# Kernel tuning notes

Measured on AMD Instinct MI355X. Metric: run time of the kernel, lower is better.

The kernel has to match this reference:

```python
import jax, jax.numpy as jnp
import numpy as np

N_HEAD = 16
N_KV_HEAD = 4
WINDOW = 256
ROPE_BASE = 10000.0


def _rotate_half(x):
    h = x.shape[-1] // 2
    return jnp.concatenate([-x[..., h:], x[..., :h]], axis=-1)


def _rope_cos_sin(T, D):
    inv_freq = 1.0 / (ROPE_BASE ** (jnp.arange(0, D, 2, dtype=jnp.float32) / D))
    t = jnp.arange(T, dtype=jnp.float32)
    freqs = t[:, None] * inv_freq[None, :]            # [T, D/2]
    emb = jnp.concatenate([freqs, freqs], axis=-1)    # [T, D]
    return jnp.cos(emb)[None, None], jnp.sin(emb)[None, None]  # [1,1,T,D]


def _masks(T, w):
    tq = jnp.arange(T)
    tk = jnp.arange(T)
    causal = tk[None, :] <= tq[:, None]
    i_blk = (tq // w) * w                              # window block start per query
    k_start = jnp.maximum(0, i_blk - w // 2)           # local key slice start
    # torch SDPA is_causal with L!=S: top-left aligned tril -> local kj <= local qi
    upper = tq - (i_blk - k_start)
    local = (tk[None, :] >= k_start[:, None]) & (tk[None, :] <= upper[:, None])
    return causal, local


def setup_inputs() -> dict:
    key = jax.random.key(0)
    k0, k1, k2, k3, k4 = jax.random.split(key, 5)
    B, T, C = 1, 2048, 2048
    D = C // N_HEAD
    s = 0.02
    return {
        "x": jax.random.normal(k0, (B, T, C), dtype=jnp.float32),
        "wq": jax.random.normal(k1, (C, N_HEAD * D), dtype=jnp.float32) * s,
        "wk": jax.random.normal(k2, (C, N_KV_HEAD * D), dtype=jnp.float32) * s,
        "wv": jax.random.normal(k3, (C, N_KV_HEAD * D), dtype=jnp.float32) * s,
        "wo": jax.random.normal(k4, (C, C), dtype=jnp.float32) * s,
    }


def reference(x, wq, wk, wv, wo):
    B, T, C = x.shape
    D = C // N_HEAD
    g = N_HEAD // N_KV_HEAD

    q = (x @ wq).reshape(B, T, N_HEAD, D)
    k = (x @ wk).reshape(B, T, N_KV_HEAD, D)
    v = (x @ wv).reshape(B, T, N_KV_HEAD, D)
    k = jnp.repeat(k, g, axis=2)                       # GQA repeat_interleave
    v = jnp.repeat(v, g, axis=2)
    q = q.transpose(0, 2, 1, 3)                        # [B,H,T,D]
    k = k.transpose(0, 2, 1, 3)
    v = v.transpose(0, 2, 1, 3)

    cos, sin = _rope_cos_sin(T, D)
    q = q * cos + _rotate_half(q) * sin
    k = k * cos + _rotate_half(k) * sin

    scale = 1.0 / jnp.sqrt(jnp.asarray(D, dtype=q.dtype))
    scores = jnp.einsum('bhqd,bhkd->bhqk', q, k) * scale
    causal, local = _masks(T, WINDOW)
    neg = jnp.finfo(scores.dtype).min
    p_g = jax.nn.softmax(jnp.where(causal, scores, neg), axis=-1)
    p_l = jax.nn.softmax(jnp.where(local, scores, neg), axis=-1)
    out_g = jnp.einsum('bhqk,bhkd->bhqd', p_g, v)
    out_l = jnp.einsum('bhqk,bhkd->bhqd', p_l, v)
    out = 0.5 * (out_g + out_l)
    out = out.transpose(0, 2, 1, 3).reshape(B, T, C)
    return out @ wo
```

## Files before the change

kernel.cpp:

```cpp
#include <hip/hip_runtime.h>
#include <hip/hip_bf16.h>
#include <cstdint>
#include <cstddef>

#define T_SEQ 2048
#define CDIM  2048
#define HQ    16
#define HKV   4
#define DHEAD 128
#define NQKV  3072

typedef __bf16 bf8 __attribute__((ext_vector_type(8)));
typedef __bf16 bf4 __attribute__((ext_vector_type(4)));
typedef float  f4  __attribute__((ext_vector_type(4)));

static __device__ __forceinline__ f4 mfma16(bf8 a, bf8 b, f4 c) {
    return __builtin_amdgcn_mfma_f32_16x16x32_bf16(a, b, c, 0, 0, 0);
}

#define GLOAD16(g, l)                                                        \
    __builtin_amdgcn_global_load_lds(                                        \
        (const __attribute__((address_space(1))) void*)(g),                  \
        (__attribute__((address_space(3))) void*)(l), 16, 0, 0)

__global__ __launch_bounds__(256) void k_pre(const float* __restrict__ x,
                                             const float* __restrict__ wq,
                                             const float* __restrict__ wk,
                                             const float* __restrict__ wv,
                                             const float* __restrict__ wo,
                                             __bf16* __restrict__ xbf,
                                             float* __restrict__ tab,
                                             __bf16* __restrict__ wqkvT,
                                             __bf16* __restrict__ woT) {
    const int bid = blockIdx.x, tid = threadIdx.x;
    if (bid < 4096) {
        int i = bid * 256 + tid;
        float4 v = ((const float4*)x)[i];
        bf4 o;
        o[0] = (__bf16)v.x; o[1] = (__bf16)v.y; o[2] = (__bf16)v.z; o[3] = (__bf16)v.w;
        ((bf4*)xbf)[i] = o;
        return;
    }
    if (bid < 4608) {
        int idx = (bid - 4096) * 256 + tid;
        int t = idx >> 6, j = idx & 63;
        float invf = expf(-(float)j * (9.210340371976184f / 64.0f));
        float a = (float)t * invf;
        tab[idx * 2 + 0] = cosf(a);
        tab[idx * 2 + 1] = sinf(a);
        return;
    }
    __shared__ float tile[32][33];
    const int n = bid - 4608;
    const int bx = n % 160, by = n / 160;
    const float* src; __bf16* dst; int ld_src, cx;
    if (bx < 64)      { src = wq; dst = wqkvT;                        ld_src = 2048; cx = bx; }
    else if (bx < 80) { src = wk; dst = wqkvT + (size_t)2048 * 2048;  ld_src = 512;  cx = bx - 64; }
    else if (bx < 96) { src = wv; dst = wqkvT + (size_t)2560 * 2048;  ld_src = 512;  cx = bx - 80; }
    else              { src = wo; dst = woT;                          ld_src = 2048; cx = bx - 96; }
    const int c0 = cx * 32, r0 = by * 32;
    const int tx = tid & 31, ty = tid >> 5;
#pragma unroll
    for (int i = 0; i < 4; ++i)
        tile[ty + i * 8][tx] = src[(size_t)(r0 + ty + i * 8) * ld_src + c0 + tx];
    __syncthreads();
#pragma unroll
    for (int i = 0; i < 4; ++i)
        dst[(size_t)(c0 + ty + i * 8) * 2048 + r0 + tx] = (__bf16)tile[tx][ty + i * 8];
}

template <int MODE>
__global__ __launch_bounds__(512, 4) void k_gemm(const __bf16* __restrict__ A,
                                                 const __bf16* __restrict__ BT,
                                                 float* __restrict__ C,
                                                 const float2* __restrict__ tab,
                                                 __bf16* __restrict__ Qo,
                                                 __bf16* __restrict__ Ko,
                                                 __bf16* __restrict__ Vo,
                                                 int M, int N, int K) {
    __shared__ __bf16 lds[2][2][128 * 64];
    char* L = (char*)&lds[0][0][0];
    const int tid = threadIdx.x, wid = tid >> 6, lane = tid & 63;
    const int l15 = lane & 15, lhi = lane >> 4;
    const int wr = wid >> 1, wc = wid & 1;
    const size_t arow0 = (size_t)blockIdx.y * 128;
    const size_t brow0 = (size_t)blockIdx.x * 128;

    const int sr = tid >> 3;
    const int sc8 = ((tid & 7) ^ ((tid >> 3) & 7)) * 8;
    const __bf16* Ag = A + (arow0 + sr) * K + sc8;
    const __bf16* Bg = BT + (brow0 + sr) * K + sc8;

#define GSTAGE(buf, k0)                                                          \
    {                                                                            \
        _Pragma("unroll") for (int i = 0; i < 2; ++i) {                          \
            GLOAD16(Ag + (k0) + (size_t)i * 64 * K,                              \
                    L + (buf) * 32768 + i * 8192 + tid * 16);                    \
            GLOAD16(Bg + (k0) + (size_t)i * 64 * K,                              \
                    L + (buf) * 32768 + 16384 + i * 8192 + tid * 16);            \
        }                                                                        \
    }

    f4 acc[2][4] = {};
    GSTAGE(0, 0);
    __syncthreads();
    int cur = 0;

    for (int k0 = 0; k0 < K; k0 += 64) {
        if (k0 + 64 < K) GSTAGE(cur ^ 1, k0 + 64);
        const char* Ab = L + cur * 32768;
        const char* Bb = Ab + 16384;
        bf8 af[2][2], bfr[2][4];
#pragma unroll
        for (int kk = 0; kk < 2; ++kk) {
            const int ch = ((kk * 4 + lhi) ^ (l15 & 7)) * 16;
#pragma unroll
            for (int m = 0; m < 2; ++m)
                af[kk][m] = *(const bf8*)(Ab + (wr * 32 + m * 16 + l15) * 128 + ch);
#pragma unroll
            for (int n = 0; n < 4; ++n)
                bfr[kk][n] = *(const bf8*)(Bb + (n * 32 + wc * 16 + l15) * 128 + ch);
        }
        __builtin_amdgcn_s_setprio(1);
#pragma unroll
        for (int kk = 0; kk < 2; ++kk)
#pragma unroll
            for (int m = 0; m < 2; ++m)
#pragma unroll
                for (int n = 0; n < 4; ++n)
                    acc[m][n] = mfma16(af[kk][m], bfr[kk][n], acc[m][n]);
        __builtin_amdgcn_s_setprio(0);
        __syncthreads();
        cur ^= 1;
    }
#undef GSTAGE

    const int row0 = blockIdx.y * 128 + wr * 32;
    if (MODE == 0) {
#pragma unroll
        for (int m = 0; m < 2; ++m)
#pragma unroll
            for (int n = 0; n < 4; ++n) {
                const int c = blockIdx.x * 128 + n * 32 + wc * 16 + l15;
#pragma unroll
                for (int j = 0; j < 4; ++j)
                    C[(size_t)(row0 + m * 16 + lhi * 4 + j) * N + c] = acc[m][n][j];
            }
    } else {
        const int bx = blockIdx.x;
        if (bx < 20) {
            __bf16* dst0 = (bx < 16) ? (Qo + (size_t)bx * T_SEQ * DHEAD)
                                     : (Ko + (size_t)(bx - 16) * T_SEQ * DHEAD);
#pragma unroll
            for (int m = 0; m < 2; ++m)
#pragma unroll
                for (int n = 0; n < 2; ++n) {
                    const int d = n * 32 + wc * 16 + l15;
#pragma unroll
                    for (int j = 0; j < 4; ++j) {
                        const int t = row0 + m * 16 + lhi * 4 + j;
                        const float2 cs = tab[t * 64 + d];
                        const float a = acc[m][n][j], b = acc[m][n + 2][j];
                        dst0[(size_t)t * DHEAD + d]      = (__bf16)(a * cs.x - b * cs.y);
                        dst0[(size_t)t * DHEAD + d + 64] = (__bf16)(b * cs.x + a * cs.y);
                    }
                }
        } else {
            __bf16* vdst = Vo + (size_t)(bx - 20) * DHEAD * T_SEQ;
#pragma unroll
            for (int m = 0; m < 2; ++m)
#pragma unroll
                for (int n = 0; n < 4; ++n) {
                    const int c = n * 32 + wc * 16 + l15;
                    bf4 o;
#pragma unroll
                    for (int j = 0; j < 4; ++j) o[j] = (__bf16)acc[m][n][j];
                    *(bf4*)&vdst[(size_t)c * T_SEQ + row0 + m * 16 + lhi * 4] = o;
                }
        }
    }
}

__global__ __launch_bounds__(512) void k_attn(const __bf16* __restrict__ Q,
                                              const __bf16* __restrict__ Kr,
                                              const __bf16* __restrict__ VT,
                                              __bf16* __restrict__ att) {
    __shared__ __align__(16) char lds[155648];
    char* KlB  = lds;
    char* VlB  = lds + 65536;
    char* PlB0 = lds + 131072;
    char* PwB0 = lds + 147456;

    const int h = blockIdx.y, kvh = h >> 2;
    const int qt = (blockIdx.y < 8) ? (31 - (int)blockIdx.x) : (int)blockIdx.x;
    const int tid = threadIdx.x, wid = tid >> 6, lane = tid & 63;
    const int l15 = lane & 15, lhi = lane >> 4;
    const int par = wid >> 2, qw = wid & 3;
    const int q0w = qt * 64 + qw * 16;
    const bool hasloc = qt >= 4;
    const int lfLo = 4 * (qt >> 2) - 2;
    const int lpart = qt - 2;
    const float CE = 0.12751741f;
    const float L2E = 1.44269504f;
    const float SCL = 0.08838834764831845f;
    const float THR = 5.5451774f;

    char* PlB = PlB0 + wid * 2048;
    char* PwB = PwB0 + qw * 2048;

    const int srow = tid >> 4;
    const int sg = (((tid & 15) ^ (srow & 15)) << 3);
    const __bf16* KgB = Kr + (size_t)kvh * T_SEQ * DHEAD;
    const __bf16* VgB = VT + (size_t)kvh * DHEAD * T_SEQ;

#define STAGE(bsel, kb2)                                                          \
    {                                                                             \
        _Pragma("unroll") for (int i = 0; i < 4; ++i) {                           \
            GLOAD16(KgB + (size_t)((kb2) + i * 32 + srow) * DHEAD + sg,           \
                    KlB + (bsel) + i * 8192 + tid * 16);                          \
            GLOAD16(VgB + (size_t)(i * 32 + srow) * T_SEQ + (kb2) + sg,           \
                    VlB + (bsel) + i * 8192 + tid * 16);                          \
        }                                                                         \
    }

    bf8 qf[4];
#pragma unroll
    for (int dc = 0; dc < 4; ++dc)
        qf[dc] = *(const bf8*)&Q[((size_t)h * T_SEQ + q0w + l15) * DHEAD + dc * 32 + lhi * 8];

    f4 oc[8] = {}, ow[8] = {};
    float mg[4], sgp[4], slp[4];
#pragma unroll
    for (int j = 0; j < 4; ++j) { mg[j] = -__builtin_inff(); sgp[j] = slp[j] = 0.f; }
    float mgmin = -__builtin_inff();

    const int R = (qt >> 1) + 1;
    STAGE(0, 0);
    __syncthreads();
    int cur = 0;

    for (int r = 0; r < R; ++r) {
        if (r + 1 < R) STAGE((cur ^ 1) * 32768, (r + 1) * 128);
        const int kt = 2 * r + par;
        if (kt <= qt) {
            const int kb = kt * 64;
            const int cb = cur * 32768;
            const int rowb = par * 64;
            f4 sc[4] = {};
            __builtin_amdgcn_s_setprio(1);
#pragma unroll
            for (int ks = 0; ks < 4; ++ks)
#pragma unroll
                for (int dc = 0; dc < 4; ++dc) {
                    bf8 kf = *(const bf8*)(KlB + cb + (rowb + ks * 16 + l15) * 256 +
                                           (((dc * 4 + lhi) ^ l15) << 4));
                    sc[ks] = mfma16(qf[dc], kf, sc[ks]);
                }
            __builtin_amdgcn_s_setprio(0);

            float t[4][4];
#pragma unroll
            for (int ks = 0; ks < 4; ++ks)
#pragma unroll
                for (int j = 0; j < 4; ++j) t[ks][j] = sc[ks][j];
            if (kt == qt) {
#pragma unroll
                for (int ks = 0; ks < 4; ++ks)
#pragma unroll
                    for (int j = 0; j < 4; ++j)
                        if (kb + ks * 16 + l15 > q0w + lhi * 4 + j) t[ks][j] = -3.0e38f;
            }
            float mx = t[0][0];
#pragma unroll
            for (int ks = 0; ks < 4; ++ks)
#pragma unroll
                for (int j = 0; j < 4; ++j) mx = fmaxf(mx, t[ks][j]);
            mx *= SCL;
            if (!__all(mx <= mgmin + THR)) {
#pragma unroll
                for (int j = 0; j < 4; ++j) {
                    float m2 = fmaxf(fmaxf(t[0][j], t[1][j]), fmaxf(t[2][j], t[3][j])) * SCL;
#pragma unroll
                    for (int x = 1; x < 16; x <<= 1) m2 = fmaxf(m2, __shfl_xor(m2, x));
                    float mn = fmaxf(mg[j], m2);
                    float f = __builtin_amdgcn_exp2f((mg[j] - mn) * L2E);
                    mg[j] = mn;
                    sgp[j] *= f; slp[j] *= f;
#pragma unroll
                    for (int nd = 0; nd < 8; ++nd) { oc[nd][j] *= f; ow[nd][j] *= f; }
                }
                mgmin = fminf(fminf(mg[0], mg[1]), fminf(mg[2], mg[3]));
            }
            float p[4][4], psum[4];
#pragma unroll
            for (int j = 0; j < 4; ++j) {
                const float bj = mg[j] * L2E;
#pragma unroll
                for (int ks = 0; ks < 4; ++ks)
                    p[ks][j] = __builtin_amdgcn_exp2f(t[ks][j] * CE - bj);
                psum[j] = (p[0][j] + p[1][j]) + (p[2][j] + p[3][j]);
                sgp[j] += psum[j];
            }
            const bool part = hasloc && (kt == lpart);
            if (!part) {
#pragma unroll
                for (int j = 0; j < 4; ++j) {
                    const int rsw = ((lhi * 4 + j) & 7) << 4;
                    const int rb = (lhi * 4 + j) * 128;
#pragma unroll
                    for (int ks = 0; ks < 4; ++ks)
                        *(__bf16*)(PlB + rb + ((ks * 32 + 2 * l15) ^ rsw)) = (__bf16)p[ks][j];
                }
            } else {
                const int e = q0w + lhi * 4 - 128 - kb - l15;
#pragma unroll
                for (int j = 0; j < 4; ++j) {
                    const int rsw = ((lhi * 4 + j) & 7) << 4;
                    const int rb = (lhi * 4 + j) * 128;
                    float lsum = 0.f;
#pragma unroll
                    for (int ks = 0; ks < 4; ++ks) {
                        float l = (ks * 16 <= e + j) ? p[ks][j] : 0.f;
                        lsum += l;
                        *(__bf16*)(PwB + rb + ((ks * 32 + 2 * l15) ^ rsw)) = (__bf16)l;
                        *(__bf16*)(PlB + rb + ((ks * 32 + 2 * l15) ^ rsw)) = (__bf16)(p[ks][j] - l);
                    }
                    slp[j] += lsum;
                }
            }
            const bool inwin = hasloc && kt >= lfLo && kt < lpart;
            if (inwin) {
#pragma unroll
                for (int j = 0; j < 4; ++j) slp[j] += psum[j];
            }
            const int psw = (l15 & 7) << 4;
            bf8 pf0 = *(const bf8*)(PlB + l15 * 128 + ((lhi << 4) ^ psw));
            bf8 pf1 = *(const bf8*)(PlB + l15 * 128 + ((64 + (lhi << 4)) ^ psw));
            const int vg0 = ((par * 8 + lhi) ^ l15) << 4;
            const int vg1 = ((par * 8 + 4 + lhi) ^ l15) << 4;
            __builtin_amdgcn_s_setprio(1);
            if (part) {
                bf8 pw0 = *(const bf8*)(PwB + l15 * 128 + ((lhi << 4) ^ psw));
                bf8 pw1 = *(const bf8*)(PwB + l15 * 128 + ((64 + (lhi << 4)) ^ psw));
#pragma unroll
                for (int nd = 0; nd < 8; ++nd) {
                    bf8 v0 = *(const bf8*)(VlB + cb + (nd * 16 + l15) * 256 + vg0);
                    bf8 v1 = *(const bf8*)(VlB + cb + (nd * 16 + l15) * 256 + vg1);
                    oc[nd] = mfma16(pf0, v0, oc[nd]);
                    oc[nd] = mfma16(pf1, v1, oc[nd]);
                    ow[nd] = mfma16(pw0, v0, ow[nd]);
                    ow[nd] = mfma16(pw1, v1, ow[nd]);
                }
            } else if (inwin) {
#pragma unroll
                for (int nd = 0; nd < 8; ++nd) {
                    bf8 v0 = *(const bf8*)(VlB + cb + (nd * 16 + l15) * 256 + vg0);
                    bf8 v1 = *(const bf8*)(VlB + cb + (nd * 16 + l15) * 256 + vg1);
                    ow[nd] = mfma16(pf0, v0, ow[nd]);
                    ow[nd] = mfma16(pf1, v1, ow[nd]);
                }
            } else {
#pragma unroll
                for (int nd = 0; nd < 8; ++nd) {
                    bf8 v0 = *(const bf8*)(VlB + cb + (nd * 16 + l15) * 256 + vg0);
                    bf8 v1 = *(const bf8*)(VlB + cb + (nd * 16 + l15) * 256 + vg1);
                    oc[nd] = mfma16(pf0, v0, oc[nd]);
                    oc[nd] = mfma16(pf1, v1, oc[nd]);
                }
            }
            __builtin_amdgcn_s_setprio(0);
        }
        __syncthreads();
        cur ^= 1;
    }

    if (par) {
        char* sb = lds + qw * 20480 + lane * 320;
#pragma unroll
        for (int nd = 0; nd < 8; ++nd) *(f4*)(sb + nd * 16) = oc[nd];
#pragma unroll
        for (int nd = 0; nd < 8; ++nd) *(f4*)(sb + 128 + nd * 16) = ow[nd];
        f4 a, b, c;
#pragma unroll
        for (int j = 0; j < 4; ++j) { a[j] = mg[j]; b[j] = sgp[j]; c[j] = slp[j]; }
        *(f4*)(sb + 256) = a; *(f4*)(sb + 272) = b; *(f4*)(sb + 288) = c;
    }
    __syncthreads();
    if (!par) {
        char* sb = lds + qw * 20480 + lane * 320;
        f4 mB = *(const f4*)(sb + 256);
        f4 sB = *(const f4*)(sb + 272);
        f4 lB = *(const f4*)(sb + 288);
        float fA[4], fB[4];
#pragma unroll
        for (int j = 0; j < 4; ++j) {
            float ms = fmaxf(mg[j], mB[j]);
            fA[j] = __builtin_amdgcn_exp2f((mg[j] - ms) * L2E);
            fB[j] = __builtin_amdgcn_exp2f((mB[j] - ms) * L2E);
            sgp[j] = sgp[j] * fA[j] + sB[j] * fB[j];
            slp[j] = slp[j] * fA[j] + lB[j] * fB[j];
        }
#pragma unroll
        for (int nd = 0; nd < 8; ++nd) {
            f4 ocB = *(const f4*)(sb + nd * 16);
            f4 owB = *(const f4*)(sb + 128 + nd * 16);
#pragma unroll
            for (int j = 0; j < 4; ++j) {
                oc[nd][j] = oc[nd][j] * fA[j] + ocB[j] * fB[j];
                ow[nd][j] = ow[nd][j] * fA[j] + owB[j] * fB[j];
            }
        }
#pragma unroll
        for (int j = 0; j < 4; ++j) {
#pragma unroll
            for (int x = 1; x < 16; x <<= 1) {
                sgp[j] += __shfl_xor(sgp[j], x);
                slp[j] += __shfl_xor(slp[j], x);
            }
        }
        float rg[4], rl[4];
#pragma unroll
        for (int j = 0; j < 4; ++j) {
            rg[j] = 1.f / sgp[j];
            rl[j] = hasloc ? 0.5f / slp[j] : 0.f;
        }
#pragma unroll
        for (int nd = 0; nd < 8; ++nd)
#pragma unroll
            for (int j = 0; j < 4; ++j) {
                int q = q0w + lhi * 4 + j;
                float go = oc[nd][j] + ow[nd][j];
                float v = hasloc ? (go * (0.5f * rg[j]) + ow[nd][j] * rl[j]) : go * rg[j];
                att[(size_t)q * CDIM + h * DHEAD + nd * 16 + l15] = (__bf16)v;
            }
    }
#undef STAGE
}

extern "C" void kernel_launch(void* const* d_in, const int* in_sizes, int n_in,
                              void* d_out, int out_size, void* d_ws, size_t ws_size,
                              hipStream_t stream) {
    const float* x  = (const float*)d_in[0];
    const float* wq = (const float*)d_in[1];
    const float* wk = (const float*)d_in[2];
    const float* wv = (const float*)d_in[3];
    const float* wo = (const float*)d_in[4];
    char* ws = (char*)d_ws;

    __bf16* xbf   = (__bf16*)(ws + 0);
    __bf16* wqkvT = (__bf16*)(ws + 8388608);
    __bf16* woT   = (__bf16*)(ws + 20971520);
    __bf16* Q     = (__bf16*)(ws + 41943040);
    __bf16* K     = (__bf16*)(ws + 50331648);
    __bf16* VTb   = (__bf16*)(ws + 52428800);
    __bf16* att   = (__bf16*)(ws + 54525952);
    float*  tab   = (float*)(ws + 62914560);

    k_pre<<<14848, 256, 0, stream>>>(x, wq, wk, wv, wo, xbf, tab, wqkvT, woT);
    k_gemm<1><<<dim3(24, 16), 512, 0, stream>>>(xbf, wqkvT, nullptr, (const float2*)tab,
                                                Q, K, VTb, 2048, 3072, 2048);
    k_attn<<<dim3(32, 16), 512, 0, stream>>>(Q, K, VTb, att);
    k_gemm<0><<<dim3(16, 16), 512, 0, stream>>>(att, woT, (float*)d_out, nullptr,
                                                nullptr, nullptr, nullptr, 2048, 2048, 2048);
}
```

Measured before the change: 138.1 us.

## Drop K/V double buffering and reuse P tile to fit two attention blocks per CU

Shrinks the attention kernel's shared memory from about 152KB to 80KB. It removes the double-buffered K/V staging, drops the separate local-window P buffer by rewriting the shared P tile for the partial-window block, and compacts the cross-wave reduction scratch. The aim is to let more blocks reside per CU, so occupancy hides latency instead of software prefetch. The change also adds a launch-bounds occupancy hint, which may cap registers and cause spills, and drops the reversed query-tile ordering that balanced the causal workload across heads.

```diff
diff --git a/kernel.cpp b/kernel.cpp
--- a/kernel.cpp
+++ b/kernel.cpp
@@ -181,18 +181,17 @@
     }
 }
 
-__global__ __launch_bounds__(512) void k_attn(const __bf16* __restrict__ Q,
-                                              const __bf16* __restrict__ Kr,
-                                              const __bf16* __restrict__ VT,
-                                              __bf16* __restrict__ att) {
-    __shared__ __align__(16) char lds[155648];
+__global__ __launch_bounds__(512, 4) void k_attn(const __bf16* __restrict__ Q,
+                                                 const __bf16* __restrict__ Kr,
+                                                 const __bf16* __restrict__ VT,
+                                                 __bf16* __restrict__ att) {
+    __shared__ __align__(16) char lds[81920];
     char* KlB  = lds;
-    char* VlB  = lds + 65536;
-    char* PlB0 = lds + 131072;
-    char* PwB0 = lds + 147456;
+    char* VlB  = lds + 32768;
+    char* PlB0 = lds + 65536;
 
     const int h = blockIdx.y, kvh = h >> 2;
-    const int qt = (blockIdx.y < 8) ? (31 - (int)blockIdx.x) : (int)blockIdx.x;
+    const int qt = (int)blockIdx.x;
     const int tid = threadIdx.x, wid = tid >> 6, lane = tid & 63;
     const int l15 = lane & 15, lhi = lane >> 4;
     const int par = wid >> 2, qw = wid & 3;
@@ -206,20 +205,19 @@
     const float THR = 5.5451774f;
 
     char* PlB = PlB0 + wid * 2048;
-    char* PwB = PwB0 + qw * 2048;
 
     const int srow = tid >> 4;
     const int sg = (((tid & 15) ^ (srow & 15)) << 3);
     const __bf16* KgB = Kr + (size_t)kvh * T_SEQ * DHEAD;
     const __bf16* VgB = VT + (size_t)kvh * DHEAD * T_SEQ;
 
-#define STAGE(bsel, kb2)                                                          \
+#define STAGE(kb2)                                                                \
     {                                                                             \
         _Pragma("unroll") for (int i = 0; i < 4; ++i) {                           \
             GLOAD16(KgB + (size_t)((kb2) + i * 32 + srow) * DHEAD + sg,           \
-                    KlB + (bsel) + i * 8192 + tid * 16);                          \
+                    KlB + i * 8192 + tid * 16);                                   \
             GLOAD16(VgB + (size_t)(i * 32 + srow) * T_SEQ + (kb2) + sg,           \
-                    VlB + (bsel) + i * 8192 + tid * 16);                          \
+                    VlB + i * 8192 + tid * 16);                                   \
         }                                                                         \
     }
 
@@ -235,16 +233,13 @@
     float mgmin = -__builtin_inff();
 
     const int R = (qt >> 1) + 1;
-    STAGE(0, 0);
-    __syncthreads();
-    int cur = 0;
 
     for (int r = 0; r < R; ++r) {
-        if (r + 1 < R) STAGE((cur ^ 1) * 32768, (r + 1) * 128);
+        STAGE(r * 128);
+        __syncthreads();
         const int kt = 2 * r + par;
         if (kt <= qt) {
             const int kb = kt * 64;
-            const int cb = cur * 32768;
             const int rowb = par * 64;
             f4 sc[4] = {};
             __builtin_amdgcn_s_setprio(1);
@@ -252,7 +247,7 @@
             for (int ks = 0; ks < 4; ++ks)
 #pragma unroll
                 for (int dc = 0; dc < 4; ++dc) {
-                    bf8 kf = *(const bf8*)(KlB + cb + (rowb + ks * 16 + l15) * 256 +
+                    bf8 kf = *(const bf8*)(KlB + (rowb + ks * 16 + l15) * 256 +
                                            (((dc * 4 + lhi) ^ l15) << 4));
                     sc[ks] = mfma16(qf[dc], kf, sc[ks]);
                 }
@@ -302,6 +297,7 @@
                 sgp[j] += psum[j];
             }
             const bool part = hasloc && (kt == lpart);
+            const int e = q0w + lhi * 4 - 128 - kb - l15;
             if (!part) {
 #pragma unroll
                 for (int j = 0; j < 4; ++j) {
@@ -312,7 +308,6 @@
                         *(__bf16*)(PlB + rb + ((ks * 32 + 2 * l15) ^ rsw)) = (__bf16)p[ks][j];
                 }
             } else {
-                const int e = q0w + lhi * 4 - 128 - kb - l15;
 #pragma unroll
                 for (int j = 0; j < 4; ++j) {
                     const int rsw = ((lhi * 4 + j) & 7) << 4;
@@ -322,7 +317,6 @@
                     for (int ks = 0; ks < 4; ++ks) {
                         float l = (ks * 16 <= e + j) ? p[ks][j] : 0.f;
                         lsum += l;
-                        *(__bf16*)(PwB + rb + ((ks * 32 + 2 * l15) ^ rsw)) = (__bf16)l;
                         *(__bf16*)(PlB + rb + ((ks * 32 + 2 * l15) ^ rsw)) = (__bf16)(p[ks][j] - l);
                     }
                     slp[j] += lsum;
@@ -340,12 +334,22 @@
             const int vg1 = ((par * 8 + 4 + lhi) ^ l15) << 4;
             __builtin_amdgcn_s_setprio(1);
             if (part) {
-                bf8 pw0 = *(const bf8*)(PwB + l15 * 128 + ((lhi << 4) ^ psw));
-                bf8 pw1 = *(const bf8*)(PwB + l15 * 128 + ((64 + (lhi << 4)) ^ psw));
+#pragma unroll
+                for (int j = 0; j < 4; ++j) {
+                    const int rsw = ((lhi * 4 + j) & 7) << 4;
+                    const int rb = (lhi * 4 + j) * 128;
+#pragma unroll
+                    for (int ks = 0; ks < 4; ++ks) {
+                        float l = (ks * 16 <= e + j) ? p[ks][j] : 0.f;
+                        *(__bf16*)(PlB + rb + ((ks * 32 + 2 * l15) ^ rsw)) = (__bf16)l;
+                    }
+                }
+                bf8 pw0 = *(const bf8*)(PlB + l15 * 128 + ((lhi << 4) ^ psw));
+                bf8 pw1 = *(const bf8*)(PlB + l15 * 128 + ((64 + (lhi << 4)) ^ psw));
 #pragma unroll
                 for (int nd = 0; nd < 8; ++nd) {
-                    bf8 v0 = *(const bf8*)(VlB + cb + (nd * 16 + l15) * 256 + vg0);
-                    bf8 v1 = *(const bf8*)(VlB + cb + (nd * 16 + l15) * 256 + vg1);
+                    bf8 v0 = *(const bf8*)(VlB + (nd * 16 + l15) * 256 + vg0);
+                    bf8 v1 = *(const bf8*)(VlB + (nd * 16 + l15) * 256 + vg1);
                     oc[nd] = mfma16(pf0, v0, oc[nd]);
                     oc[nd] = mfma16(pf1, v1, oc[nd]);
                     ow[nd] = mfma16(pw0, v0, ow[nd]);
@@ -354,16 +358,16 @@
             } else if (inwin) {
 #pragma unroll
                 for (int nd = 0; nd < 8; ++nd) {
-                    bf8 v0 = *(const bf8*)(VlB + cb + (nd * 16 + l15) * 256 + vg0);
-                    bf8 v1 = *(const bf8*)(VlB + cb + (nd * 16 + l15) * 256 + vg1);
+                    bf8 v0 = *(const bf8*)(VlB + (nd * 16 + l15) * 256 + vg0);
+                    bf8 v1 = *(const bf8*)(VlB + (nd * 16 + l15) * 256 + vg1);
                     ow[nd] = mfma16(pf0, v0, ow[nd]);
                     ow[nd] = mfma16(pf1, v1, ow[nd]);
                 }
             } else {
 #pragma unroll
                 for (int nd = 0; nd < 8; ++nd) {
-                    bf8 v0 = *(const bf8*)(VlB + cb + (nd * 16 + l15) * 256 + vg0);
-                    bf8 v1 = *(const bf8*)(VlB + cb + (nd * 16 + l15) * 256 + vg1);
+                    bf8 v0 = *(const bf8*)(VlB + (nd * 16 + l15) * 256 + vg0);
+                    bf8 v1 = *(const bf8*)(VlB + (nd * 16 + l15) * 256 + vg1);
                     oc[nd] = mfma16(pf0, v0, oc[nd]);
                     oc[nd] = mfma16(pf1, v1, oc[nd]);
                 }
@@ -371,11 +375,10 @@
             __builtin_amdgcn_s_setprio(0);
         }
         __syncthreads();
-        cur ^= 1;
-    }
-
+    }
+
+    char* sb = lds + (size_t)(qw * 64 + lane) * 304;
     if (par) {
-        char* sb = lds + qw * 20480 + lane * 320;
 #pragma unroll
         for (int nd = 0; nd < 8; ++nd) *(f4*)(sb + nd * 16) = oc[nd];
 #pragma unroll
@@ -387,7 +390,6 @@
     }
     __syncthreads();
     if (!par) {
-        char* sb = lds + qw * 20480 + lane * 320;
         f4 mB = *(const f4*)(sb + 256);
         f4 sB = *(const f4*)(sb + 272);
         f4 lB = *(const f4*)(sb + 288);
```

Result: slower. 192.1 us (+39.0%).
